# Performance work log

Hardware: AMD Instinct MI355X
Metric: run time of the kernel (lower is better)

The kernel has to match this reference:

```python
import jax, jax.numpy as jnp
import numpy as np

# graph layout constants
B = 64        # number of graphs
NPG = 512     # nodes per graph
N = B * NPG   # total nodes
DEG = 16      # avg degree
E = N * DEG   # total edges
F_IN = 256
H, C = 4, 64  # heads, per-head dim
K = NPG // 2  # topk pooling keeps ratio=0.5 per graph


def setup_inputs() -> dict:
    key = jax.random.key(0)
    ks = jax.random.split(key, 8)
    x = jax.random.normal(ks[0], (N, F_IN), dtype=jnp.float32)
    # within-graph random edges (src -> dst), contiguous node ids per graph
    offs = jnp.repeat(jnp.arange(B, dtype=jnp.int64) * NPG, NPG * DEG)
    src = offs + jax.random.randint(ks[1], (E,), 0, NPG)
    dst = offs + jax.random.randint(ks[2], (E,), 0, NPG)
    edge_index = jnp.stack([src, dst]).astype(jnp.int64)
    W = jax.random.normal(ks[3], (F_IN, H, C), dtype=jnp.float32) / np.sqrt(F_IN)
    att_src = jax.random.normal(ks[4], (H, C), dtype=jnp.float32) / np.sqrt(C)
    att_dst = jax.random.normal(ks[5], (H, C), dtype=jnp.float32) / np.sqrt(C)
    bias = jnp.zeros((H * C,), dtype=jnp.float32)
    bn_gamma = jnp.ones((H * C,), dtype=jnp.float32)
    bn_beta = jnp.zeros((H * C,), dtype=jnp.float32)
    pool_weight = jax.random.normal(ks[6], (H * C,), dtype=jnp.float32) / np.sqrt(H * C)
    return {"x": x, "edge_index": edge_index, "W": W, "att_src": att_src,
            "att_dst": att_dst, "bias": bias, "bn_gamma": bn_gamma,
            "bn_beta": bn_beta, "pool_weight": pool_weight}


def reference(x, edge_index, W, att_src, att_dst, bias, bn_gamma, bn_beta, pool_weight):
    n = x.shape[0]
    # --- GATConv ---
    h = jnp.einsum('nf,fhc->nhc', x, W)                 # [N,H,C]
    a_src = jnp.sum(h * att_src, axis=-1)               # [N,H]
    a_dst = jnp.sum(h * att_dst, axis=-1)               # [N,H]
    loops = jnp.arange(n, dtype=edge_index.dtype)        # add_self_loops=True default
    src = jnp.concatenate([edge_index[0], loops])
    dst = jnp.concatenate([edge_index[1], loops])
    e = jax.nn.leaky_relu(a_src[src] + a_dst[dst], 0.2)  # [E+N,H]
    # scatter-softmax over edges grouped by destination node
    emax = jax.ops.segment_max(e, dst, num_segments=n)
    ex = jnp.exp(e - emax[dst])
    den = jax.ops.segment_sum(ex, dst, num_segments=n)
    alpha = ex / (den[dst] + 1e-16)                      # [E+N,H]
    msg = alpha[:, :, None] * h[src]                     # [E+N,H,C]
    out = jax.ops.segment_sum(msg, dst, num_segments=n)  # [N,H,C]
    feat = out.reshape(n, H * C) + bias                  # concat heads
    # --- ReLU + BatchNorm (batch stats, training mode) ---
    feat = jax.nn.relu(feat)
    mean = jnp.mean(feat, axis=0)
    var = jnp.var(feat, axis=0)
    feat = (feat - mean) * jax.lax.rsqrt(var + 1e-5) * bn_gamma + bn_beta
    # --- TopKPooling (score = x.w/||w||, keep top ratio per graph, gate by tanh) ---
    score = feat @ pool_weight / jnp.linalg.norm(pool_weight)  # [N]
    top_s, top_i = jax.lax.top_k(score.reshape(B, NPG), K)     # [B,K]
    fg = feat.reshape(B, NPG, H * C)
    sel = jnp.take_along_axis(fg, top_i[:, :, None], axis=1)    # [B,K,HC]
    pooled = sel * jnp.tanh(top_s)[:, :, None]
    return pooled.reshape(B * K, H * C)
```

## Files before the change

### kernel.cpp

```cpp
#include <hip/hip_runtime.h>
#include <math.h>

#define N_NODES 32768
#define NPG 512
#define NGRAPH 64
#define KKEEP 256
#define CAP 64

typedef __attribute__((ext_vector_type(8))) short short8;
typedef __attribute__((ext_vector_type(4))) float f32x4;

__device__ __forceinline__ unsigned short f2bf(float v) {
  unsigned u = __builtin_bit_cast(unsigned, v);
  u = (u + 0x7FFFu + ((u >> 16) & 1u)) >> 16;
  return (unsigned short)u;
}
__device__ __forceinline__ float bf2f(unsigned short u) {
  unsigned v = ((unsigned)u) << 16;
  return __builtin_bit_cast(float, v);
}

__device__ __forceinline__ void async_cp16(unsigned short* l, const unsigned short* g) {
  __builtin_amdgcn_global_load_lds(
      (const __attribute__((address_space(1))) unsigned int*)g,
      (__attribute__((address_space(3))) unsigned int*)l, 16, 0, 0);
}

__global__ __launch_bounds__(256) void k_conv(
    const float* __restrict__ W,
    unsigned short* __restrict__ wth, unsigned short* __restrict__ wtl,
    unsigned short* __restrict__ wtll) {
  const int t = threadIdx.x;
  int n = blockIdx.x * 4 + (t >> 6);
  int k = (t & 63) * 4;
  unsigned short hb[4], lb[4], qb[4];
#pragma unroll
  for (int j = 0; j < 4; j++) {
    float v = W[(size_t)(k + j) * 256 + n];
    unsigned short hh = f2bf(v);
    float e1 = v - bf2f(hh);
    unsigned short ll = f2bf(e1);
    float e2 = e1 - bf2f(ll);
    hb[j] = hh; lb[j] = ll; qb[j] = f2bf(e2);
  }
  *(uint2*)&wth[(size_t)n * 256 + k] = *(uint2*)&hb[0];
  *(uint2*)&wtl[(size_t)n * 256 + k] = *(uint2*)&lb[0];
  *(uint2*)&wtll[(size_t)n * 256 + k] = *(uint2*)&qb[0];
}

#define A_STR 65
#define B_BASE 6240
__global__ __launch_bounds__(256) void k_gemm_hist(
    const float* __restrict__ x,
    const unsigned short* __restrict__ wth, const unsigned short* __restrict__ wtl,
    const unsigned short* __restrict__ wtll,
    const float* __restrict__ attS, const float* __restrict__ attD,
    float* __restrict__ h, float* __restrict__ a_src, float* __restrict__ a_dst,
    const int* __restrict__ ei, int E, int* __restrict__ cnt,
    unsigned short* __restrict__ nbr) {
  __shared__ unsigned short lds[18528];
  const int t = threadIdx.x;
  const int bid = blockIdx.x;
  if (bid >= 1024) {
    int e = (bid - 1024) * 256 + t;
    if (e < E) {
      int s = ei[e];
      int d = ei[E + e];
      int slot = atomicAdd(&cnt[d], 1);
      if (slot < CAP) nbr[(size_t)d * CAP + slot] = (unsigned short)(s & (NPG - 1));
    }
    return;
  }
  const int mb = (bid & 7) * 64 + (bid >> 4);
  const int nh = (bid >> 3) & 1;
  const int row0 = mb * 64;
  const int wid = t >> 6, lane = t & 63;
  const int q = lane >> 4, ln = lane & 15;
  const int wm = (wid >> 1) * 32, wn = (wid & 1) * 64;
  f32x4 acc[2][4] = {};

  for (int kc = 0; kc < 8; kc++) {
    const int k0 = kc * 32;
#pragma unroll
    for (int i = 0; i < 2; i++) {
      int u = i * 256 + t;
      int cq = u >> 7, r = u & 127;
      size_t gb = (size_t)(nh * 128 + r) * 256 + k0 + cq * 8;
      async_cp16(&lds[B_BASE + 0 * 4096 + u * 8], &wth[gb]);
      async_cp16(&lds[B_BASE + 1 * 4096 + u * 8], &wtl[gb]);
      async_cp16(&lds[B_BASE + 2 * 4096 + u * 8], &wtll[gb]);
    }
    {
      int r = t >> 2, cq = t & 3;
      size_t ga = (size_t)(row0 + r) * 256 + k0 + cq * 8;
      float4 f0 = *(const float4*)&x[ga];
      float4 f1 = *(const float4*)&x[ga + 4];
      float ff[8] = {f0.x, f0.y, f0.z, f0.w, f1.x, f1.y, f1.z, f1.w};
      unsigned short hs[8], ls[8], qs[8];
#pragma unroll
      for (int j = 0; j < 8; j++) {
        unsigned short hh = f2bf(ff[j]);
        float e1 = ff[j] - bf2f(hh);
        unsigned short ll = f2bf(e1);
        float e2 = e1 - bf2f(ll);
        hs[j] = hh; ls[j] = ll; qs[j] = f2bf(e2);
      }
      *(uint4*)&lds[((0 * 4 + cq) * A_STR + r) * 8] = *(uint4*)&hs[0];
      *(uint4*)&lds[((1 * 4 + cq) * A_STR + r) * 8] = *(uint4*)&ls[0];
      *(uint4*)&lds[((2 * 4 + cq) * A_STR + r) * 8] = *(uint4*)&qs[0];
    }
    __syncthreads();
    short8 ah[2], al[2], aq[2];
#pragma unroll
    for (int mt = 0; mt < 2; mt++) {
      int r = wm + mt * 16 + ln;
      ah[mt] = *(const short8*)&lds[((0 * 4 + q) * A_STR + r) * 8];
      al[mt] = *(const short8*)&lds[((1 * 4 + q) * A_STR + r) * 8];
      aq[mt] = *(const short8*)&lds[((2 * 4 + q) * A_STR + r) * 8];
    }
#pragma unroll
    for (int nt = 0; nt < 4; nt++) {
      int r = wn + nt * 16 + ln;
      short8 bh = *(const short8*)&lds[B_BASE + 0 * 4096 + (q * 128 + r) * 8];
      short8 bl = *(const short8*)&lds[B_BASE + 1 * 4096 + (q * 128 + r) * 8];
      short8 bq = *(const short8*)&lds[B_BASE + 2 * 4096 + (q * 128 + r) * 8];
#pragma unroll
      for (int mt = 0; mt < 2; mt++) {
        acc[mt][nt] = __builtin_amdgcn_mfma_f32_16x16x32_bf16(ah[mt], bh, acc[mt][nt], 0, 0, 0);
        acc[mt][nt] = __builtin_amdgcn_mfma_f32_16x16x32_bf16(ah[mt], bl, acc[mt][nt], 0, 0, 0);
        acc[mt][nt] = __builtin_amdgcn_mfma_f32_16x16x32_bf16(al[mt], bh, acc[mt][nt], 0, 0, 0);
        acc[mt][nt] = __builtin_amdgcn_mfma_f32_16x16x32_bf16(ah[mt], bq, acc[mt][nt], 0, 0, 0);
        acc[mt][nt] = __builtin_amdgcn_mfma_f32_16x16x32_bf16(al[mt], bl, acc[mt][nt], 0, 0, 0);
        acc[mt][nt] = __builtin_amdgcn_mfma_f32_16x16x32_bf16(aq[mt], bh, acc[mt][nt], 0, 0, 0);
      }
    }
    __syncthreads();
  }
  const int head = nh * 2 + (wid & 1);
  float sA[4], sD[4];
#pragma unroll
  for (int nt = 0; nt < 4; nt++) {
    int n = nh * 128 + wn + nt * 16 + ln;
    sA[nt] = attS[n];
    sD[nt] = attD[n];
  }
  float2* epi = (float2*)lds;
#pragma unroll
  for (int mt = 0; mt < 2; mt++) {
#pragma unroll
    for (int reg = 0; reg < 4; reg++) {
      int m = row0 + wm + mt * 16 + q * 4 + reg;
      float ps = 0.f, pd = 0.f;
#pragma unroll
      for (int nt = 0; nt < 4; nt++) {
        float v = acc[mt][nt][reg];
        h[(size_t)m * 256 + nh * 128 + wn + nt * 16 + ln] = v;
        ps = fmaf(v, sA[nt], ps);
        pd = fmaf(v, sD[nt], pd);
      }
      epi[(((wid * 4 + q) * 8) + mt * 4 + reg) * 18 + (ln ^ (q * 4))] =
          make_float2(ps, pd);
    }
  }
  __syncthreads();
  if (lane < 32) {
    const int rr2 = lane & 7;
    const int q2 = lane >> 3;
    const int base = (((wid * 4 + q2) * 8) + rr2) * 18;
    float ps = 0.f, pd = 0.f;
#pragma unroll
    for (int i = 0; i < 16; i++) {
      float2 v = epi[base + (i ^ (q2 * 4))];
      ps += v.x;
      pd += v.y;
    }
    int m = row0 + wm + (rr2 >> 2) * 16 + q2 * 4 + (rr2 & 3);
    a_src[m * 4 + head] = ps;
    a_dst[m * 4 + head] = pd;
  }
}

__global__ __launch_bounds__(256) void k_agg(
    const float* __restrict__ h, const float* __restrict__ a_src,
    const float* __restrict__ a_dst, const int* __restrict__ cnt,
    const unsigned short* __restrict__ nbr, const float* __restrict__ bias,
    float* __restrict__ feat) {
  __shared__ float p_lds[4][68][4];
  __shared__ int s_lds[4][68];
  const int wv = threadIdx.x >> 6;
  const int lane = threadIdx.x & 63;
  int nb = (blockIdx.x & 7) * (N_NODES / 4 / 8) + (blockIdx.x >> 3);
  const int node = nb * 4 + wv;
  const int head = lane >> 4;
  const int li = lane & 15;
  const int c0 = lane * 4;
  const int base = node & ~(NPG - 1);
  const float ad = a_dst[node * 4 + head];
  int n = cnt[node];
  if (n > CAP) n = CAP;
  float e_reg[5];
  int srcs[5];
  int nit = 0;
  float m = -1e30f;
  for (int j = li; j <= n; j += 16) {
    int s = (j < n) ? base + (int)nbr[(size_t)node * CAP + j] : node;
    float e = a_src[s * 4 + head] + ad;
    e = (e > 0.f) ? e : 0.2f * e;
    srcs[nit] = s;
    e_reg[nit++] = e;
    m = fmaxf(m, e);
  }
#pragma unroll
  for (int d = 1; d < 16; d <<= 1) m = fmaxf(m, __shfl_xor(m, d, 16));
  float l = 0.f;
  for (int i = 0; i < nit; i++) {
    int j = li + i * 16;
    float p = __expf(e_reg[i] - m);
    l += p;
    p_lds[wv][j][head] = p;
    if (head == 0) s_lds[wv][j] = srcs[i];
  }
#pragma unroll
  for (int d = 1; d < 16; d <<= 1) l += __shfl_xor(l, d, 16);
  const float linv = 1.f / (l + 1e-16f);
  __builtin_amdgcn_s_waitcnt(0);
  float4 acc0 = make_float4(0.f, 0.f, 0.f, 0.f);
  float4 acc1 = make_float4(0.f, 0.f, 0.f, 0.f);
  int j = 0;
  for (; j + 1 <= n; j += 2) {
    float p0 = p_lds[wv][j][head];
    float p1 = p_lds[wv][j + 1][head];
    int s0 = s_lds[wv][j];
    int s1 = s_lds[wv][j + 1];
    float4 h0 = *(const float4*)&h[(size_t)s0 * 256 + c0];
    float4 h1 = *(const float4*)&h[(size_t)s1 * 256 + c0];
    acc0.x = fmaf(p0, h0.x, acc0.x); acc1.x = fmaf(p1, h1.x, acc1.x);
    acc0.y = fmaf(p0, h0.y, acc0.y); acc1.y = fmaf(p1, h1.y, acc1.y);
    acc0.z = fmaf(p0, h0.z, acc0.z); acc1.z = fmaf(p1, h1.z, acc1.z);
    acc0.w = fmaf(p0, h0.w, acc0.w); acc1.w = fmaf(p1, h1.w, acc1.w);
  }
  if (j <= n) {
    float p0 = p_lds[wv][j][head];
    int s0 = s_lds[wv][j];
    float4 h0 = *(const float4*)&h[(size_t)s0 * 256 + c0];
    acc0.x = fmaf(p0, h0.x, acc0.x);
    acc0.y = fmaf(p0, h0.y, acc0.y);
    acc0.z = fmaf(p0, h0.z, acc0.z);
    acc0.w = fmaf(p0, h0.w, acc0.w);
  }
  const float4 b4 = *(const float4*)&bias[c0];
  float4 o;
  o.x = fmaxf(fmaf(acc0.x + acc1.x, linv, b4.x), 0.f);
  o.y = fmaxf(fmaf(acc0.y + acc1.y, linv, b4.y), 0.f);
  o.z = fmaxf(fmaf(acc0.z + acc1.z, linv, b4.z), 0.f);
  o.w = fmaxf(fmaf(acc0.w + acc1.w, linv, b4.w), 0.f);
  *(float4*)&feat[(size_t)node * 256 + c0] = o;
}

__global__ __launch_bounds__(256) void k_bn_partial(const float* __restrict__ feat,
                                                    double* __restrict__ psum,
                                                    double* __restrict__ psq) {
  const int c = threadIdx.x;
  const int r0 = blockIdx.x * 128;
  double s = 0.0, q = 0.0;
  for (int i = 0; i < 128; i++) {
    double v = (double)feat[(size_t)(r0 + i) * 256 + c];
    s += v;
    q += v * v;
  }
  psum[blockIdx.x * 256 + c] = s;
  psq[blockIdx.x * 256 + c] = q;
}

__global__ __launch_bounds__(1024) void k_bn_final(
    const double* __restrict__ psum, const double* __restrict__ psq,
    const float* __restrict__ gam, const float* __restrict__ bet,
    const float* __restrict__ pw, float* __restrict__ cA, float* __restrict__ cB,
    float* __restrict__ sv) {
  __shared__ double reds[4][256];
  __shared__ double redq[4][256];
  __shared__ double wsq[256];
  __shared__ double sb[256];
  const int t = threadIdx.x;
  const int c = t & 255, sl = t >> 8;
  double s = 0.0, q = 0.0;
  for (int i = sl * 64; i < sl * 64 + 64; i++) {
    s += psum[i * 256 + c];
    q += psq[i * 256 + c];
  }
  reds[sl][c] = s;
  redq[sl][c] = q;
  if (sl == 0) {
    double w = (double)pw[c];
    wsq[c] = w * w;
  }
  __syncthreads();
  if (t == 0) {
    double nn = 0.0;
    for (int i = 0; i < 256; i++) nn += wsq[i];
    wsq[0] = sqrt(nn);
  }
  __syncthreads();
  if (sl == 0) {
    s = reds[0][c] + reds[1][c] + reds[2][c] + reds[3][c];
    q = redq[0][c] + redq[1][c] + redq[2][c] + redq[3][c];
    double mean = s / (double)N_NODES;
    double var = q / (double)N_NODES - mean * mean;
    double a = (double)gam[c] / sqrt(var + 1e-5);
    double cb = (double)bet[c] - mean * a;
    cA[c] = (float)a;
    cB[c] = (float)cb;
    double pwnv = (double)pw[c] / wsq[0];
    sv[c] = (float)(a * pwnv);
    sb[c] = cb * pwnv;
  }
  __syncthreads();
  if (t == 0) {
    double s0 = 0.0;
    for (int i = 0; i < 256; i++) s0 += sb[i];
    sv[256] = (float)s0;
  }
}

__global__ __launch_bounds__(256) void k_score(
    const float* __restrict__ feat, const float* __restrict__ sv,
    float* __restrict__ score) {
  const int lane = threadIdx.x & 63;
  const int node = blockIdx.x * 4 + (threadIdx.x >> 6);
  const int c0 = lane * 4;
  float4 f = *(const float4*)&feat[(size_t)node * 256 + c0];
  float4 w = *(const float4*)&sv[c0];
  float p = f.x * w.x + f.y * w.y + f.z * w.z + f.w * w.w;
#pragma unroll
  for (int d = 1; d < 64; d <<= 1) p += __shfl_xor(p, d, 64);
  if (lane == 0) score[node] = p + sv[256];
}

__global__ __launch_bounds__(256) void k_topk(
    const float* __restrict__ score, const float* __restrict__ feat,
    const float* __restrict__ cA, const float* __restrict__ cB,
    float* __restrict__ out) {
  __shared__ float ss[NPG];
  __shared__ int rnk[64];
  __shared__ float gt[64];
  const int g = blockIdx.x >> 3;
  const int part = blockIdx.x & 7;
  const int t = threadIdx.x;
  ss[t] = score[g * NPG + t];
  ss[t + 256] = score[g * NPG + t + 256];
  __syncthreads();
  const int ln = t & 3;
  const int ndl = part * 64 + (t >> 2);
  const float s = ss[ndl];
  int rank = 0;
  for (int j = ln * 128; j < ln * 128 + 128; j++) {
    float sj = ss[j];
    rank += (sj > s || (sj == s && j < ndl)) ? 1 : 0;
  }
  rank += __shfl_xor(rank, 1);
  rank += __shfl_xor(rank, 2);
  if (ln == 0) {
    rnk[t >> 2] = rank;
    gt[t >> 2] = tanhf(s);
  }
  __syncthreads();
  for (int idx = t; idx < 64 * 64; idx += 256) {
    int r = idx >> 6;
    int rank2 = rnk[r];
    if (rank2 < KKEEP) {
      int c4 = (idx & 63) * 4;
      int node = g * NPG + part * 64 + r;
      float4 f = *(const float4*)&feat[(size_t)node * 256 + c4];
      float4 a = *(const float4*)&cA[c4];
      float4 b = *(const float4*)&cB[c4];
      float tg = gt[r];
      float4 o;
      o.x = fmaf(f.x, a.x, b.x) * tg;
      o.y = fmaf(f.y, a.y, b.y) * tg;
      o.z = fmaf(f.z, a.z, b.z) * tg;
      o.w = fmaf(f.w, a.w, b.w) * tg;
      *(float4*)&out[(size_t)(g * KKEEP + rank2) * 256 + c4] = o;
    }
  }
}

extern "C" void kernel_launch(void* const* d_in, const int* in_sizes, int n_in,
                              void* d_out, int out_size, void* d_ws, size_t ws_size,
                              hipStream_t stream) {
  const float* x    = (const float*)d_in[0];
  const int*   ei   = (const int*)d_in[1];
  const float* W    = (const float*)d_in[2];
  const float* attS = (const float*)d_in[3];
  const float* attD = (const float*)d_in[4];
  const float* bias = (const float*)d_in[5];
  const float* gam  = (const float*)d_in[6];
  const float* bet  = (const float*)d_in[7];
  const float* pw   = (const float*)d_in[8];
  float* out = (float*)d_out;
  const int E = in_sizes[1] / 2;

  char* p = (char*)d_ws;
  float* h     = (float*)p; p += (size_t)N_NODES * 256 * 4;
  float* feat  = (float*)p; p += (size_t)N_NODES * 256 * 4;
  float* a_src = (float*)p; p += (size_t)N_NODES * 4 * 4;
  float* a_dst = (float*)p; p += (size_t)N_NODES * 4 * 4;
  float* score = (float*)p; p += (size_t)N_NODES * 4;
  double* psum = (double*)p; p += (size_t)256 * 256 * 8;
  double* psq  = (double*)p; p += (size_t)256 * 256 * 8;
  float* cA    = (float*)p; p += 256 * 4;
  float* cB    = (float*)p; p += 256 * 4;
  float* sv    = (float*)p; p += 260 * 4;
  unsigned short* wth  = (unsigned short*)p; p += (size_t)256 * 256 * 2;
  unsigned short* wtl  = (unsigned short*)p; p += (size_t)256 * 256 * 2;
  unsigned short* wtll = (unsigned short*)p; p += (size_t)256 * 256 * 2;
  int* cnt     = (int*)p;   p += (size_t)N_NODES * 4;
  unsigned short* nbr = (unsigned short*)p; p += (size_t)N_NODES * CAP * 2;

  hipMemsetAsync(cnt, 0, (size_t)N_NODES * 4, stream);
  k_conv<<<64, 256, 0, stream>>>(W, wth, wtl, wtll);
  k_gemm_hist<<<3072, 256, 0, stream>>>(x, wth, wtl, wtll, attS, attD,
                                        h, a_src, a_dst, ei, E, cnt, nbr);
  k_agg<<<N_NODES / 4, 256, 0, stream>>>(h, a_src, a_dst, cnt, nbr, bias, feat);
  k_bn_partial<<<256, 256, 0, stream>>>(feat, psum, psq);
  k_bn_final<<<1, 1024, 0, stream>>>(psum, psq, gam, bet, pw, cA, cB, sv);
  k_score<<<N_NODES / 4, 256, 0, stream>>>(feat, sv, score);
  k_topk<<<NGRAPH * 8, 256, 0, stream>>>(score, feat, cA, cB, out);
}
```

Measured before the change: 221.9 us.

## Double-buffer weight tiles and prefetch x in 512-thread GEMM blocks

The fused GEMM+histogram kernel now runs 512-thread blocks that each compute a 128-row tile instead of 64 rows, so every weight slice loaded into LDS is reused by twice as many rows. The three bf16 weight splits are double-buffered: the next K-chunk is copied asynchronously while MFMAs run on the current one. The next x chunk is prefetched into registers and split into bf16 parts during compute, which replaces the previous two-sync-per-chunk serial load/compute pattern. This costs more LDS per block (about 74 KB) and more threads per block, which may lower occupancy. The epilogue's use of LDS with the larger tile is not fully visible here.

Result: faster. 203.7 us (-8.2%).

```diff
diff --git a/kernel.cpp b/kernel.cpp
--- a/kernel.cpp
+++ b/kernel.cpp
@@ -24,6 +24,16 @@
   __builtin_amdgcn_global_load_lds(
       (const __attribute__((address_space(1))) unsigned int*)g,
       (__attribute__((address_space(3))) unsigned int*)l, 16, 0, 0);
+}
+
+__device__ __forceinline__ void block_barrier() {
+  __builtin_amdgcn_sched_barrier(0);
+  asm volatile("s_barrier" ::: "memory");
+  __builtin_amdgcn_sched_barrier(0);
+}
+__device__ __forceinline__ void wait_all() {
+  asm volatile("s_waitcnt vmcnt(0) lgkmcnt(0)" ::: "memory");
+  __builtin_amdgcn_sched_barrier(0);
 }
 
 __global__ __launch_bounds__(256) void k_conv(
@@ -48,9 +58,11 @@
   *(uint2*)&wtll[(size_t)n * 256 + k] = *(uint2*)&qb[0];
 }
 
-#define A_STR 65
-#define B_BASE 6240
-__global__ __launch_bounds__(256) void k_gemm_hist(
+#define A_STR 129
+#define A_SZ 12384
+#define B_BASE 12384
+#define B_SZ 12288
+__global__ __launch_bounds__(512, 4) void k_gemm_hist(
     const float* __restrict__ x,
     const unsigned short* __restrict__ wth, const unsigned short* __restrict__ wtl,
     const unsigned short* __restrict__ wtll,
@@ -58,11 +70,11 @@
     float* __restrict__ h, float* __restrict__ a_src, float* __restrict__ a_dst,
     const int* __restrict__ ei, int E, int* __restrict__ cnt,
     unsigned short* __restrict__ nbr) {
-  __shared__ unsigned short lds[18528];
+  __shared__ unsigned short lds[36960];
   const int t = threadIdx.x;
   const int bid = blockIdx.x;
-  if (bid >= 1024) {
-    int e = (bid - 1024) * 256 + t;
+  if (bid >= 512) {
+    int e = (bid - 512) * 512 + t;
     if (e < E) {
       int s = ei[e];
       int d = ei[E + e];
@@ -71,45 +83,55 @@
     }
     return;
   }
-  const int mb = (bid & 7) * 64 + (bid >> 4);
+  const int mb = (bid & 7) * 32 + (bid >> 4);
   const int nh = (bid >> 3) & 1;
-  const int row0 = mb * 64;
+  const int row0 = mb * 128;
   const int wid = t >> 6, lane = t & 63;
   const int q = lane >> 4, ln = lane & 15;
   const int wm = (wid >> 1) * 32, wn = (wid & 1) * 64;
+  const int sr = t >> 2, scq = t & 3;
   f32x4 acc[2][4] = {};
 
+  {
+    size_t ga = (size_t)(row0 + sr) * 256 + scq * 8;
+    float4 f0 = *(const float4*)&x[ga];
+    float4 f1 = *(const float4*)&x[ga + 4];
+    float ff[8] = {f0.x, f0.y, f0.z, f0.w, f1.x, f1.y, f1.z, f1.w};
+    unsigned short hs[8], ls[8], qs[8];
+#pragma unroll
+    for (int j = 0; j < 8; j++) {
+      unsigned short hh = f2bf(ff[j]);
+      float e1 = ff[j] - bf2f(hh);
+      unsigned short ll = f2bf(e1);
+      float e2 = e1 - bf2f(ll);
+      hs[j] = hh; ls[j] = ll; qs[j] = f2bf(e2);
+    }
+    *(uint4*)&lds[((0 * 4 + scq) * A_STR + sr) * 8] = *(uint4*)&hs[0];
+    *(uint4*)&lds[((1 * 4 + scq) * A_STR + sr) * 8] = *(uint4*)&ls[0];
+    *(uint4*)&lds[((2 * 4 + scq) * A_STR + sr) * 8] = *(uint4*)&qs[0];
+    size_t gb = (size_t)(nh * 128 + (t & 127)) * 256 + (t >> 7) * 8;
+    async_cp16(&lds[B_BASE + 0 * 4096 + t * 8], &wth[gb]);
+    async_cp16(&lds[B_BASE + 1 * 4096 + t * 8], &wtl[gb]);
+    async_cp16(&lds[B_BASE + 2 * 4096 + t * 8], &wtll[gb]);
+  }
+  wait_all();
+  block_barrier();
+
   for (int kc = 0; kc < 8; kc++) {
-    const int k0 = kc * 32;
-#pragma unroll
-    for (int i = 0; i < 2; i++) {
-      int u = i * 256 + t;
-      int cq = u >> 7, r = u & 127;
-      size_t gb = (size_t)(nh * 128 + r) * 256 + k0 + cq * 8;
-      async_cp16(&lds[B_BASE + 0 * 4096 + u * 8], &wth[gb]);
-      async_cp16(&lds[B_BASE + 1 * 4096 + u * 8], &wtl[gb]);
-      async_cp16(&lds[B_BASE + 2 * 4096 + u * 8], &wtll[gb]);
-    }
-    {
-      int r = t >> 2, cq = t & 3;
-      size_t ga = (size_t)(row0 + r) * 256 + k0 + cq * 8;
-      float4 f0 = *(const float4*)&x[ga];
-      float4 f1 = *(const float4*)&x[ga + 4];
-      float ff[8] = {f0.x, f0.y, f0.z, f0.w, f1.x, f1.y, f1.z, f1.w};
-      unsigned short hs[8], ls[8], qs[8];
-#pragma unroll
-      for (int j = 0; j < 8; j++) {
-        unsigned short hh = f2bf(ff[j]);
-        float e1 = ff[j] - bf2f(hh);
-        unsigned short ll = f2bf(e1);
-        float e2 = e1 - bf2f(ll);
-        hs[j] = hh; ls[j] = ll; qs[j] = f2bf(e2);
-      }
-      *(uint4*)&lds[((0 * 4 + cq) * A_STR + r) * 8] = *(uint4*)&hs[0];
-      *(uint4*)&lds[((1 * 4 + cq) * A_STR + r) * 8] = *(uint4*)&ls[0];
-      *(uint4*)&lds[((2 * 4 + cq) * A_STR + r) * 8] = *(uint4*)&qs[0];
-    }
-    __syncthreads();
+    const int cur = kc & 1;
+    float4 f0, f1;
+    if (kc < 7) {
+      const int k1 = (kc + 1) * 32;
+      size_t ga = (size_t)(row0 + sr) * 256 + k1 + scq * 8;
+      f0 = *(const float4*)&x[ga];
+      f1 = *(const float4*)&x[ga + 4];
+      unsigned short* bb = &lds[B_BASE + (cur ^ 1) * B_SZ];
+      size_t gb = (size_t)(nh * 128 + (t & 127)) * 256 + k1 + (t >> 7) * 8;
+      async_cp16(&bb[0 * 4096 + t * 8], &wth[gb]);
+      async_cp16(&bb[1 * 4096 + t * 8], &wtl[gb]);
+      async_cp16(&bb[2 * 4096 + t * 8], &wtll[gb]);
+    }
+    const unsigned short* bc = &lds[B_BASE + cur * B_SZ];
     short8 ah[2], al[2], aq[2];
 #pragma unroll
     for (int mt = 0; mt < 2; mt++) {
@@ -121,9 +143,9 @@
 #pragma unroll
     for (int nt = 0; nt < 4; nt++) {
       int r = wn + nt * 16 + ln;
-      short8 bh = *(const short8*)&lds[B_BASE + 0 * 4096 + (q * 128 + r) * 8];
-      short8 bl = *(const short8*)&lds[B_BASE + 1 * 4096 + (q * 128 + r) * 8];
-      short8 bq = *(const short8*)&lds[B_BASE + 2 * 4096 + (q * 128 + r) * 8];
+      short8 bh = *(const short8*)&bc[0 * 4096 + (q * 128 + r) * 8];
+      short8 bl = *(const short8*)&bc[1 * 4096 + (q * 128 + r) * 8];
+      short8 bq = *(const short8*)&bc[2 * 4096 + (q * 128 + r) * 8];
 #pragma unroll
       for (int mt = 0; mt < 2; mt++) {
         acc[mt][nt] = __builtin_amdgcn_mfma_f32_16x16x32_bf16(ah[mt], bh, acc[mt][nt], 0, 0, 0);
@@ -134,8 +156,28 @@
         acc[mt][nt] = __builtin_amdgcn_mfma_f32_16x16x32_bf16(aq[mt], bh, acc[mt][nt], 0, 0, 0);
       }
     }
-    __syncthreads();
-  }
+    unsigned short hs[8], ls[8], qs[8];
+    if (kc < 7) {
+      float ff[8] = {f0.x, f0.y, f0.z, f0.w, f1.x, f1.y, f1.z, f1.w};
+#pragma unroll
+      for (int j = 0; j < 8; j++) {
+        unsigned short hh = f2bf(ff[j]);
+        float e1 = ff[j] - bf2f(hh);
+        unsigned short ll = f2bf(e1);
+        float e2 = e1 - bf2f(ll);
+        hs[j] = hh; ls[j] = ll; qs[j] = f2bf(e2);
+      }
+    }
+    block_barrier();
+    if (kc < 7) {
+      *(uint4*)&lds[((0 * 4 + scq) * A_STR + sr) * 8] = *(uint4*)&hs[0];
+      *(uint4*)&lds[((1 * 4 + scq) * A_STR + sr) * 8] = *(uint4*)&ls[0];
+      *(uint4*)&lds[((2 * 4 + scq) * A_STR + sr) * 8] = *(uint4*)&qs[0];
+    }
+    wait_all();
+    block_barrier();
+  }
+
   const int head = nh * 2 + (wid & 1);
   float sA[4], sD[4];
 #pragma unroll
@@ -418,7 +460,7 @@
 
   hipMemsetAsync(cnt, 0, (size_t)N_NODES * 4, stream);
   k_conv<<<64, 256, 0, stream>>>(W, wth, wtl, wtll);
-  k_gemm_hist<<<3072, 256, 0, stream>>>(x, wth, wtl, wtll, attS, attD,
+  k_gemm_hist<<<1536, 512, 0, stream>>>(x, wth, wtl, wtll, attS, attD,
                                         h, a_src, a_dst, ei, E, cnt, nbr);
   k_agg<<<N_NODES / 4, 256, 0, stream>>>(h, a_src, a_dst, cnt, nbr, bias, feat);
   k_bn_partial<<<256, 256, 0, stream>>>(feat, psum, psq);
```
